# Performance work log

Measured on AMD Instinct MI355X. Metric: run time of the kernel, lower is better.

Reference implementation:

```python
import jax, jax.numpy as jnp
import numpy as np

HEADS = 8
DIM_HEAD = 64
ROT_DIM = DIM_HEAD // 2  # RotaryEmbedding(dim=head_dim//2) rotates first 32 dims of each head
THETA = 10000.0


def _rope_cos_sin(T, dtype):
    # rotary_embedding_torch: freqs = 1/theta**(arange(0,dim,2)/dim), len dim//2,
    # angles repeated interleaved across pairs -> (T, ROT_DIM)
    inv = 1.0 / (THETA ** (jnp.arange(0, ROT_DIM, 2, dtype=jnp.float32) / ROT_DIM))
    ang = jnp.arange(T, dtype=jnp.float32)[:, None] * inv[None, :]      # (T, ROT_DIM/2)
    ang = jnp.repeat(ang, 2, axis=-1)                                   # (T, ROT_DIM) interleaved
    return jnp.cos(ang).astype(dtype), jnp.sin(ang).astype(dtype)


def _rotate_half(x):
    # pairs (x1, x2) -> (-x2, x1), interleaved layout '... (d 2)'
    x = x.reshape(x.shape[:-1] + (-1, 2))
    x = jnp.stack([-x[..., 1], x[..., 0]], axis=-1)
    return x.reshape(x.shape[:-2] + (-1,))


def _apply_rope(x, cos, sin):
    # x: (N, h, T, dh); rotate first ROT_DIM dims, pass through the rest
    xr, xp = x[..., :ROT_DIM], x[..., ROT_DIM:]
    xr = xr * cos[None, None, :, :] + _rotate_half(xr) * sin[None, None, :, :]
    return jnp.concatenate([xr, xp], axis=-1)


def setup_inputs() -> dict:
    key = jax.random.key(0)
    k1, k2, k3 = jax.random.split(key, 3)
    B, T, H, W, D = 2, 32, 32, 32, 512
    inner = HEADS * DIM_HEAD
    x = jax.random.normal(k1, (B, T, H, W, D), dtype=jnp.float32)
    w_qkv = jax.random.normal(k2, (D, 3 * inner), dtype=jnp.float32) * (D ** -0.5)
    w_out = jax.random.normal(k3, (inner, D), dtype=jnp.float32) * (inner ** -0.5)
    b_out = jnp.zeros((D,), dtype=jnp.float32)
    return {"x": x, "w_qkv": w_qkv, "w_out": w_out, "b_out": b_out}


def reference(x, w_qkv, w_out, b_out):
    B, T, H, W, D = x.shape
    qkv = jnp.einsum('bthwd,de->bthwe', x, w_qkv)               # (B,T,H,W,3*inner)
    q, k, v = jnp.split(qkv, 3, axis=-1)

    def to_axial(t):  # (B,T,H,W,inner) -> (B*H*W, heads, T, dh)
        t = t.reshape(B, T, H, W, HEADS, DIM_HEAD)
        t = jnp.transpose(t, (0, 2, 3, 4, 1, 5))
        return t.reshape(B * H * W, HEADS, T, DIM_HEAD)

    q, k, v = to_axial(q), to_axial(k), to_axial(v)
    cos, sin = _rope_cos_sin(T, x.dtype)
    q = _apply_rope(q, cos, sin)
    k = _apply_rope(k, cos, sin)

    scale = DIM_HEAD ** -0.5
    scores = jnp.einsum('nhqd,nhkd->nhqk', q, k) * scale        # (N,h,T,T)
    causal = jnp.tril(jnp.ones((T, T), dtype=bool))
    scores = jnp.where(causal[None, None, :, :], scores, jnp.finfo(scores.dtype).min)
    attn = jax.nn.softmax(scores, axis=-1)
    out = jnp.einsum('nhqk,nhkd->nhqd', attn, v)                # (N,h,T,dh)

    out = out.reshape(B, H, W, HEADS, T, DIM_HEAD)
    out = jnp.transpose(out, (0, 4, 1, 2, 3, 5)).reshape(B, T, H, W, HEADS * DIM_HEAD)
    return jnp.einsum('bthwe,ed->bthwd', out, w_out) + b_out
```

## Files before the change

kernel.cpp:

```cpp
#include <hip/hip_runtime.h>
#include <hip/hip_bf16.h>
#include <math.h>

#define HEADS  8
#define TT     32
#define DMODEL 512
#define HWSZ   1024
#define TSTRIDE (HWSZ*DMODEL)

#define NQKV (3*DMODEL*DMODEL)
#define NOUT (DMODEL*DMODEL)
#define NTAB 512

typedef __attribute__((ext_vector_type(8)))  short bf16x8;
typedef __attribute__((ext_vector_type(4)))  float f32x4;
typedef __attribute__((ext_vector_type(16))) float f32x16;
typedef __attribute__((ext_vector_type(4)))  short s16x4;

__device__ __forceinline__ unsigned short f2bf(float f) {
    unsigned int u = __builtin_bit_cast(unsigned int, f);
    u += 0x7FFFu + ((u >> 16) & 1u);
    return (unsigned short)(u >> 16);
}

__global__ __launch_bounds__(256)
void taa_prep(const float* __restrict__ wqkv, const float* __restrict__ wout,
              unsigned short* __restrict__ ws) {
    long i = (long)blockIdx.x * 256 + threadIdx.x;
    unsigned short* wqf = ws;
    unsigned short* wof = ws + NQKV;
    float* cs = (float*)(wof + NOUT);
    float* sn = cs + NTAB;
    if (i < NQKV) {
        int i8 = (int)(i & 7), lane = (int)((i >> 3) & 63), blk = (int)(i >> 9);
        int k05 = blk & 15, t = blk >> 4;
        int n = t * 16 + (lane & 15);
        int k = k05 * 32 + (lane >> 4) * 8 + i8;
        wqf[i] = f2bf(wqkv[(long)k * 1536 + n]);
    } else if (i < NQKV + NOUT) {
        long j = i - NQKV;
        int i8 = (int)(j & 7), lane = (int)((j >> 3) & 63), blk = (int)(j >> 9);
        int k05 = blk & 15, t = blk >> 4;
        int col = t * 16 + (lane & 15);
        int k = k05 * 32 + (lane >> 4) * 8 + i8;
        wof[j] = f2bf(wout[(long)k * 512 + col]);
    } else if (i < NQKV + NOUT + NTAB) {
        int j = (int)(i - NQKV - NOUT);
        int t = j >> 4, f = j & 15;
        float inv = powf(10000.f, -(float)(2 * f) / 32.f);
        float sv, cv;
        sincosf((float)t * inv, &sv, &cv);
        cs[j] = cv; sn[j] = sv;
    }
}

#define X_OFF  0
#define Q_OFF  65536
#define K_OFF  81920
#define V_OFF  98304
#define PV_OFF 114688
#define CS_OFF 131072
#define SN_OFF 133120
#define LDS_SZ 135168

#define XS(g, r, cB) (X_OFF + ((g) << 15) + ((r) << 10) + ((cB) ^ (((r) & 7) << 4)))
#define RS(base, r, cB) ((base) + ((r) << 7) + ((cB) ^ (((r) & 7) << 4)))
#define VS(base, d, cB) ((base) + ((d) << 6) + ((cB) ^ (((d) & 7) << 3)))

#define MFMA16(a, b, c) __builtin_amdgcn_mfma_f32_16x16x32_bf16((a), (b), (c), 0, 0, 0)
#define MFMA32(a, b, c) __builtin_amdgcn_mfma_f32_32x32x16_bf16((a), (b), (c), 0, 0, 0)

__global__ __launch_bounds__(512, 1)
void taa_main(const float* __restrict__ x,
              const unsigned short* __restrict__ ws,
              const float* __restrict__ b_out,
              float* __restrict__ out) {
    extern __shared__ __align__(16) unsigned char smem[];

    const unsigned short* wqf = ws;
    const unsigned short* wof = ws + NQKV;
    const float* cs_gl = (const float*)(wof + NOUT);
    const float* sn_gl = cs_gl + NTAB;

    const int tid  = threadIdx.x;
    const int lane = tid & 63;
    const int wv   = tid >> 6;
    const int quad = lane >> 4;
    const int lid  = lane & 15;

    const int n0 = blockIdx.x * 2;
    const long long base0 = ((long long)(n0 >> 10) * (TT * HWSZ) + (n0 & 1023)) * DMODEL;
    const int n1 = n0 + 1;
    const long long base1 = ((long long)(n1 >> 10) * (TT * HWSZ) + (n1 & 1023)) * DMODEL;

    float* cs_l = (float*)(smem + CS_OFF);
    float* sn_l = (float*)(smem + SN_OFF);
    for (int i = tid; i < NTAB; i += 512) { cs_l[i] = cs_gl[i]; sn_l[i] = sn_gl[i]; }

    for (int idx = tid; idx < 4096; idx += 512) {
        int g  = idx >> 11;
        int r  = (idx >> 6) & 31;
        int c8 = idx & 63;
        long long bg = g ? base1 : base0;
        const float4* src = (const float4*)(x + bg + (long long)r * TSTRIDE + c8 * 8);
        float4 f0 = src[0], f1 = src[1];
        s16x4 lo, hi;
        lo[0] = (short)f2bf(f0.x); lo[1] = (short)f2bf(f0.y);
        lo[2] = (short)f2bf(f0.z); lo[3] = (short)f2bf(f0.w);
        hi[0] = (short)f2bf(f1.x); hi[1] = (short)f2bf(f1.y);
        hi[2] = (short)f2bf(f1.z); hi[3] = (short)f2bf(f1.w);
        int a = XS(g, r, c8 * 16);
        *(s16x4*)(smem + a)     = lo;
        *(s16x4*)(smem + a + 8) = hi;
    }

    f32x4 oacc[4][2][2];
    #pragma unroll
    for (int j = 0; j < 4; ++j)
        #pragma unroll
        for (int g = 0; g < 2; ++g)
            #pragma unroll
            for (int mt = 0; mt < 2; ++mt) oacc[j][g][mt] = (f32x4){0.f, 0.f, 0.f, 0.f};

    __syncthreads();

    for (int it = 0; it < 4; ++it) {
        const int hpair = it * 2;

        for (int rnd = 0; rnd < 3; ++rnd) {
            int ct  = rnd * 8 + wv;
            int m   = ct >> 3;
            int hh  = (ct >> 2) & 1;
            int t16 = ct & 3;
            int T   = m * 32 + (hpair + hh) * 4 + t16;
            const unsigned short* wp = wqf + ((long)T * 16) * 512 + lane * 8;
            f32x4 acc[2][2];
            #pragma unroll
            for (int g = 0; g < 2; ++g)
                #pragma unroll
                for (int mt = 0; mt < 2; ++mt) acc[g][mt] = (f32x4){0.f, 0.f, 0.f, 0.f};
            #pragma unroll 4
            for (int k05 = 0; k05 < 16; ++k05) {
                bf16x8 bw = *(const bf16x8*)(wp + (long)k05 * 512);
                #pragma unroll
                for (int g = 0; g < 2; ++g)
                    #pragma unroll
                    for (int mt = 0; mt < 2; ++mt) {
                        bf16x8 a = *(const bf16x8*)(smem + XS(g, lid + 16 * mt, k05 * 64 + quad * 16));
                        acc[g][mt] = MFMA16(a, bw, acc[g][mt]);
                    }
            }
            if (m < 2) {
                int dstb = ((m == 0) ? Q_OFF : K_OFF) + hh * 4096;
                if (t16 < 2) {
                    #pragma unroll
                    for (int g = 0; g < 2; ++g)
                        #pragma unroll
                        for (int mt = 0; mt < 2; ++mt)
                            #pragma unroll
                            for (int r = 0; r < 4; ++r) {
                                float v = acc[g][mt][r];
                                float p = __shfl_xor(v, 1, 64);
                                int trow = mt * 16 + quad * 4 + r;
                                int colh = t16 * 16 + lid;
                                int jj = colh >> 1;
                                float cv = cs_l[trow * 16 + jj];
                                float sv = sn_l[trow * 16 + jj];
                                float res = (colh & 1) ? (v * cv + p * sv) : (v * cv - p * sv);
                                *(unsigned short*)(smem + RS(dstb + g * 8192, trow, colh * 2)) = f2bf(res);
                            }
                } else {
                    #pragma unroll
                    for (int g = 0; g < 2; ++g)
                        #pragma unroll
                        for (int mt = 0; mt < 2; ++mt)
                            #pragma unroll
                            for (int r = 0; r < 4; ++r) {
                                int trow = mt * 16 + quad * 4 + r;
                                *(unsigned short*)(smem + RS(dstb + g * 8192, trow, (t16 * 16 + lid) * 2)) = f2bf(acc[g][mt][r]);
                            }
                }
            } else {
                #pragma unroll
                for (int g = 0; g < 2; ++g)
                    #pragma unroll
                    for (int mt = 0; mt < 2; ++mt) {
                        int d  = t16 * 16 + lid;
                        int t0 = mt * 16 + quad * 4;
                        s16x4 pk;
                        pk[0] = (short)f2bf(acc[g][mt][0]); pk[1] = (short)f2bf(acc[g][mt][1]);
                        pk[2] = (short)f2bf(acc[g][mt][2]); pk[3] = (short)f2bf(acc[g][mt][3]);
                        *(s16x4*)(smem + VS(V_OFF + (g * 2 + hh) * 4096, d, t0 * 2)) = pk;
                    }
            }
        }
        __syncthreads();

        {
            int g  = wv >> 2;
            int hh = (wv >> 1) & 1;
            int dt = wv & 1;
            int qr  = Q_OFF  + (g * 2 + hh) * 4096;
            int kr  = K_OFF  + (g * 2 + hh) * 4096;
            int vr  = V_OFF  + (g * 2 + hh) * 4096;
            int pvr = PV_OFF + (g * 2 + hh) * 4096;
            int tq = lane & 31;
            int hf = lane >> 5;

            f32x16 sc = {0.f,0.f,0.f,0.f,0.f,0.f,0.f,0.f,0.f,0.f,0.f,0.f,0.f,0.f,0.f,0.f};
            #pragma unroll
            for (int j = 0; j < 4; ++j) {
                bf16x8 aK = *(const bf16x8*)(smem + RS(kr, tq, j * 32 + hf * 16));
                bf16x8 bQ = *(const bf16x8*)(smem + RS(qr, tq, j * 32 + hf * 16));
                sc = MFMA32(aK, bQ, sc);
            }
            float pe[16];
            float mx = -1e30f;
            #pragma unroll
            for (int r = 0; r < 16; ++r) {
                int tk = (r & 3) + 8 * (r >> 2) + 4 * hf;
                float v = (tk <= tq) ? sc[r] * 0.125f : -1e30f;
                pe[r] = v;
                mx = fmaxf(mx, v);
            }
            mx = fmaxf(mx, __shfl_xor(mx, 32, 64));
            float sum = 0.f;
            #pragma unroll
            for (int r = 0; r < 16; ++r) {
                float e = __expf(pe[r] - mx);
                pe[r] = e;
                sum += e;
            }
            sum += __shfl_xor(sum, 32, 64);
            float inv = 1.f / sum;
            bf16x8 pa0, pa1;
            #pragma unroll
            for (int i = 0; i < 8; ++i) {
                pa0[i] = (short)f2bf(pe[i] * inv);
                pa1[i] = (short)f2bf(pe[8 + i] * inv);
            }
            int d = dt * 32 + tq;
            f32x16 o = {0.f,0.f,0.f,0.f,0.f,0.f,0.f,0.f,0.f,0.f,0.f,0.f,0.f,0.f,0.f,0.f};
            {
                s16x4 lo = *(const s16x4*)(smem + VS(vr, d, 8 * hf));
                s16x4 hi = *(const s16x4*)(smem + VS(vr, d, 16 + 8 * hf));
                bf16x8 bv;
                bv[0] = lo[0]; bv[1] = lo[1]; bv[2] = lo[2]; bv[3] = lo[3];
                bv[4] = hi[0]; bv[5] = hi[1]; bv[6] = hi[2]; bv[7] = hi[3];
                o = MFMA32(pa0, bv, o);
            }
            {
                s16x4 lo = *(const s16x4*)(smem + VS(vr, d, 32 + 8 * hf));
                s16x4 hi = *(const s16x4*)(smem + VS(vr, d, 48 + 8 * hf));
                bf16x8 bv;
                bv[0] = lo[0]; bv[1] = lo[1]; bv[2] = lo[2]; bv[3] = lo[3];
                bv[4] = hi[0]; bv[5] = hi[1]; bv[6] = hi[2]; bv[7] = hi[3];
                o = MFMA32(pa1, bv, o);
            }
            #pragma unroll
            for (int r = 0; r < 16; ++r) {
                int t = (r & 3) + 8 * (r >> 2) + 4 * hf;
                *(unsigned short*)(smem + RS(pvr, t, 2 * d)) = f2bf(o[r]);
            }
        }
        __syncthreads();

        {
            #pragma unroll
            for (int k05h = 0; k05h < 4; ++k05h) {
                int hh   = k05h >> 1;
                int dblk = k05h & 1;
                int kb   = (hpair + hh) * 2 + dblk;
                bf16x8 a[2][2];
                #pragma unroll
                for (int g = 0; g < 2; ++g)
                    #pragma unroll
                    for (int mt = 0; mt < 2; ++mt)
                        a[g][mt] = *(const bf16x8*)(smem + RS(PV_OFF + (g * 2 + hh) * 4096, lid + 16 * mt, dblk * 64 + quad * 16));
                #pragma unroll
                for (int j = 0; j < 4; ++j) {
                    int ct = wv + 8 * j;
                    bf16x8 bw = *(const bf16x8*)(wof + ((long)(ct * 16 + kb)) * 512 + lane * 8);
                    #pragma unroll
                    for (int g = 0; g < 2; ++g)
                        #pragma unroll
                        for (int mt = 0; mt < 2; ++mt)
                            oacc[j][g][mt] = MFMA16(a[g][mt], bw, oacc[j][g][mt]);
                }
            }
        }
    }

    #pragma unroll
    for (int j = 0; j < 4; ++j) {
        int col = (wv + 8 * j) * 16 + lid;
        float bias = b_out[col];
        #pragma unroll
        for (int g = 0; g < 2; ++g) {
            long long bg = g ? base1 : base0;
            #pragma unroll
            for (int mt = 0; mt < 2; ++mt)
                #pragma unroll
                for (int r = 0; r < 4; ++r) {
                    int t = mt * 16 + quad * 4 + r;
                    out[bg + (long long)t * TSTRIDE + col] = oacc[j][g][mt][r] + bias;
                }
        }
    }
}

extern "C" void kernel_launch(void* const* d_in, const int* in_sizes, int n_in,
                              void* d_out, int out_size, void* d_ws, size_t ws_size,
                              hipStream_t stream) {
    const float* x     = (const float*)d_in[0];
    const float* w_qkv = (const float*)d_in[1];
    const float* w_out = (const float*)d_in[2];
    const float* b_out = (const float*)d_in[3];
    float* out = (float*)d_out;
    (void)in_sizes; (void)n_in; (void)out_size; (void)ws_size;

    unsigned short* ws = (unsigned short*)d_ws;

    taa_prep<<<dim3(4098), dim3(256), 0, stream>>>(w_qkv, w_out, ws);
    taa_main<<<dim3(1024), dim3(512), LDS_SZ, stream>>>(x, ws, b_out, out);
}
```

Baseline: 239.4 us.

## Switch QKV and output projections to 32x32 MFMA with per-wave head ownership

The QKV and output projections move from 16x16x32 MFMA tiles to 32x32x16 MFMA tiles, and the prepacked weight layout changes to match. Each wave now computes Q, K and V for one head, sample and d-half, sharing one A-fragment load across three MFMAs. Work is no longer spread over three rounds of mixed tiles. The PV buffer is relaid so the output projection reads a contiguous 32-row tile, and the launch-bounds occupancy hint rises to 2. The aim is fewer LDS A-operand loads per MFMA and less per-round bookkeeping, at the cost of larger f32x16 accumulators and more register pressure.

```diff
diff --git a/kernel.cpp b/kernel.cpp
--- a/kernel.cpp
+++ b/kernel.cpp
@@ -13,7 +13,6 @@
 #define NTAB 512
 
 typedef __attribute__((ext_vector_type(8)))  short bf16x8;
-typedef __attribute__((ext_vector_type(4)))  float f32x4;
 typedef __attribute__((ext_vector_type(16))) float f32x16;
 typedef __attribute__((ext_vector_type(4)))  short s16x4;
 
@@ -21,6 +20,11 @@
     unsigned int u = __builtin_bit_cast(unsigned int, f);
     u += 0x7FFFu + ((u >> 16) & 1u);
     return (unsigned short)(u >> 16);
+}
+
+__device__ __forceinline__ f32x16 fz16() {
+    f32x16 v = {0.f,0.f,0.f,0.f,0.f,0.f,0.f,0.f,0.f,0.f,0.f,0.f,0.f,0.f,0.f,0.f};
+    return v;
 }
 
 __global__ __launch_bounds__(256)
@@ -33,17 +37,17 @@
     float* sn = cs + NTAB;
     if (i < NQKV) {
         int i8 = (int)(i & 7), lane = (int)((i >> 3) & 63), blk = (int)(i >> 9);
-        int k05 = blk & 15, t = blk >> 4;
-        int n = t * 16 + (lane & 15);
-        int k = k05 * 32 + (lane >> 4) * 8 + i8;
+        int ks = blk & 31, ct = blk >> 5;
+        int n = ct * 32 + (lane & 31);
+        int k = ks * 16 + (lane >> 5) * 8 + i8;
         wqf[i] = f2bf(wqkv[(long)k * 1536 + n]);
     } else if (i < NQKV + NOUT) {
         long j = i - NQKV;
         int i8 = (int)(j & 7), lane = (int)((j >> 3) & 63), blk = (int)(j >> 9);
-        int k05 = blk & 15, t = blk >> 4;
-        int col = t * 16 + (lane & 15);
-        int k = k05 * 32 + (lane >> 4) * 8 + i8;
-        wof[j] = f2bf(wout[(long)k * 512 + col]);
+        int ks = blk & 31, ct = blk >> 5;
+        int n = ct * 32 + (lane & 31);
+        int k = ks * 16 + (lane >> 5) * 8 + i8;
+        wof[j] = f2bf(wout[(long)k * 512 + n]);
     } else if (i < NQKV + NOUT + NTAB) {
         int j = (int)(i - NQKV - NOUT);
         int t = j >> 4, f = j & 15;
@@ -63,14 +67,14 @@
 #define SN_OFF 133120
 #define LDS_SZ 135168
 
-#define XS(g, r, cB) (X_OFF + ((g) << 15) + ((r) << 10) + ((cB) ^ (((r) & 7) << 4)))
-#define RS(base, r, cB) ((base) + ((r) << 7) + ((cB) ^ (((r) & 7) << 4)))
-#define VS(base, d, cB) ((base) + ((d) << 6) + ((cB) ^ (((d) & 7) << 3)))
-
-#define MFMA16(a, b, c) __builtin_amdgcn_mfma_f32_16x16x32_bf16((a), (b), (c), 0, 0, 0)
+#define XS(g,r,cB) (X_OFF + ((g)<<15) + ((r)<<10) + ((cB) ^ (((r)&7)<<4)))
+#define RS(base,r,cB) ((base) + ((r)<<7) + ((cB) ^ (((r)&7)<<4)))
+#define VS(base,d,cB) ((base) + ((d)<<6) + ((cB) ^ (((d)&7)<<3)))
+#define PS(g,r,cB) (PV_OFF + ((g)<<13) + ((r)<<8) + ((cB) ^ (((r)&7)<<4)))
+
 #define MFMA32(a, b, c) __builtin_amdgcn_mfma_f32_32x32x16_bf16((a), (b), (c), 0, 0, 0)
 
-__global__ __launch_bounds__(512, 1)
+__global__ __launch_bounds__(512, 2)
 void taa_main(const float* __restrict__ x,
               const unsigned short* __restrict__ ws,
               const float* __restrict__ b_out,
@@ -85,8 +89,8 @@
     const int tid  = threadIdx.x;
     const int lane = tid & 63;
     const int wv   = tid >> 6;
-    const int quad = lane >> 4;
-    const int lid  = lane & 15;
+    const int hf   = lane >> 5;
+    const int tq   = lane & 31;
 
     const int n0 = blockIdx.x * 2;
     const long long base0 = ((long long)(n0 >> 10) * (TT * HWSZ) + (n0 & 1023)) * DMODEL;
@@ -114,100 +118,76 @@
         *(s16x4*)(smem + a + 8) = hi;
     }
 
-    f32x4 oacc[4][2][2];
-    #pragma unroll
-    for (int j = 0; j < 4; ++j)
-        #pragma unroll
-        for (int g = 0; g < 2; ++g)
-            #pragma unroll
-            for (int mt = 0; mt < 2; ++mt) oacc[j][g][mt] = (f32x4){0.f, 0.f, 0.f, 0.f};
+    f32x16 oac[2][2];
+    oac[0][0] = fz16(); oac[0][1] = fz16();
+    oac[1][0] = fz16(); oac[1][1] = fz16();
 
     __syncthreads();
 
+    const int g  = wv >> 2;
+    const int hh = (wv >> 1) & 1;
+    const int dh = wv & 1;
+
     for (int it = 0; it < 4; ++it) {
-        const int hpair = it * 2;
-
-        for (int rnd = 0; rnd < 3; ++rnd) {
-            int ct  = rnd * 8 + wv;
-            int m   = ct >> 3;
-            int hh  = (ct >> 2) & 1;
-            int t16 = ct & 3;
-            int T   = m * 32 + (hpair + hh) * 4 + t16;
-            const unsigned short* wp = wqf + ((long)T * 16) * 512 + lane * 8;
-            f32x4 acc[2][2];
-            #pragma unroll
-            for (int g = 0; g < 2; ++g)
+        const int hd = it * 2 + hh;
+
+        const unsigned short* pq = wqf + ((long)((      hd * 2 + dh) * 32)) * 512 + lane * 8;
+        const unsigned short* pk = wqf + ((long)((16 + hd * 2 + dh) * 32)) * 512 + lane * 8;
+        const unsigned short* pv = wqf + ((long)((32 + hd * 2 + dh) * 32)) * 512 + lane * 8;
+        f32x16 aq = fz16(), ak = fz16(), av = fz16();
+        #pragma unroll 4
+        for (int ks = 0; ks < 32; ++ks) {
+            bf16x8 a   = *(const bf16x8*)(smem + XS(g, tq, ks * 32 + hf * 16));
+            bf16x8 wq_ = *(const bf16x8*)(pq + (long)ks * 512);
+            bf16x8 wk_ = *(const bf16x8*)(pk + (long)ks * 512);
+            bf16x8 wv_ = *(const bf16x8*)(pv + (long)ks * 512);
+            aq = MFMA32(a, wq_, aq);
+            ak = MFMA32(a, wk_, ak);
+            av = MFMA32(a, wv_, av);
+        }
+        {
+            int qb = Q_OFF + (g * 2 + hh) * 4096;
+            int kb = K_OFF + (g * 2 + hh) * 4096;
+            if (dh == 0) {
                 #pragma unroll
-                for (int mt = 0; mt < 2; ++mt) acc[g][mt] = (f32x4){0.f, 0.f, 0.f, 0.f};
-            #pragma unroll 4
-            for (int k05 = 0; k05 < 16; ++k05) {
-                bf16x8 bw = *(const bf16x8*)(wp + (long)k05 * 512);
-                #pragma unroll
-                for (int g = 0; g < 2; ++g)
-                    #pragma unroll
-                    for (int mt = 0; mt < 2; ++mt) {
-                        bf16x8 a = *(const bf16x8*)(smem + XS(g, lid + 16 * mt, k05 * 64 + quad * 16));
-                        acc[g][mt] = MFMA16(a, bw, acc[g][mt]);
-                    }
-            }
-            if (m < 2) {
-                int dstb = ((m == 0) ? Q_OFF : K_OFF) + hh * 4096;
-                if (t16 < 2) {
-                    #pragma unroll
-                    for (int g = 0; g < 2; ++g)
-                        #pragma unroll
-                        for (int mt = 0; mt < 2; ++mt)
-                            #pragma unroll
-                            for (int r = 0; r < 4; ++r) {
-                                float v = acc[g][mt][r];
-                                float p = __shfl_xor(v, 1, 64);
-                                int trow = mt * 16 + quad * 4 + r;
-                                int colh = t16 * 16 + lid;
-                                int jj = colh >> 1;
-                                float cv = cs_l[trow * 16 + jj];
-                                float sv = sn_l[trow * 16 + jj];
-                                float res = (colh & 1) ? (v * cv + p * sv) : (v * cv - p * sv);
-                                *(unsigned short*)(smem + RS(dstb + g * 8192, trow, colh * 2)) = f2bf(res);
-                            }
-                } else {
-                    #pragma unroll
-                    for (int g = 0; g < 2; ++g)
-                        #pragma unroll
-                        for (int mt = 0; mt < 2; ++mt)
-                            #pragma unroll
-                            for (int r = 0; r < 4; ++r) {
-                                int trow = mt * 16 + quad * 4 + r;
-                                *(unsigned short*)(smem + RS(dstb + g * 8192, trow, (t16 * 16 + lid) * 2)) = f2bf(acc[g][mt][r]);
-                            }
+                for (int r = 0; r < 16; ++r) {
+                    int t = (r & 3) + 8 * (r >> 2) + 4 * hf;
+                    float cv = cs_l[t * 16 + (tq >> 1)];
+                    float sv = sn_l[t * 16 + (tq >> 1)];
+                    float vq = aq[r], pq2 = __shfl_xor(vq, 1, 64);
+                    float rq = (tq & 1) ? (vq * cv + pq2 * sv) : (vq * cv - pq2 * sv);
+                    *(unsigned short*)(smem + RS(qb, t, tq * 2)) = f2bf(rq);
+                    float vk = ak[r], pk2 = __shfl_xor(vk, 1, 64);
+                    float rk = (tq & 1) ? (vk * cv + pk2 * sv) : (vk * cv - pk2 * sv);
+                    *(unsigned short*)(smem + RS(kb, t, tq * 2)) = f2bf(rk);
                 }
             } else {
                 #pragma unroll
-                for (int g = 0; g < 2; ++g)
-                    #pragma unroll
-                    for (int mt = 0; mt < 2; ++mt) {
-                        int d  = t16 * 16 + lid;
-                        int t0 = mt * 16 + quad * 4;
-                        s16x4 pk;
-                        pk[0] = (short)f2bf(acc[g][mt][0]); pk[1] = (short)f2bf(acc[g][mt][1]);
-                        pk[2] = (short)f2bf(acc[g][mt][2]); pk[3] = (short)f2bf(acc[g][mt][3]);
-                        *(s16x4*)(smem + VS(V_OFF + (g * 2 + hh) * 4096, d, t0 * 2)) = pk;
-                    }
+                for (int r = 0; r < 16; ++r) {
+                    int t = (r & 3) + 8 * (r >> 2) + 4 * hf;
+                    *(unsigned short*)(smem + RS(qb, t, 64 + tq * 2)) = f2bf(aq[r]);
+                    *(unsigned short*)(smem + RS(kb, t, 64 + tq * 2)) = f2bf(ak[r]);
+                }
+            }
+            int vb = V_OFF + (g * 2 + hh) * 4096;
+            int d  = dh * 32 + tq;
+            #pragma unroll
+            for (int c = 0; c < 4; ++c) {
+                s16x4 pkk;
+                pkk[0] = (short)f2bf(av[c * 4 + 0]);
+                pkk[1] = (short)f2bf(av[c * 4 + 1]);
+                pkk[2] = (short)f2bf(av[c * 4 + 2]);
+                pkk[3] = (short)f2bf(av[c * 4 + 3]);
+                *(s16x4*)(smem + VS(vb, d, c * 16 + hf * 8)) = pkk;
             }
         }
         __syncthreads();
 
         {
-            int g  = wv >> 2;
-            int hh = (wv >> 1) & 1;
-            int dt = wv & 1;
-            int qr  = Q_OFF  + (g * 2 + hh) * 4096;
-            int kr  = K_OFF  + (g * 2 + hh) * 4096;
-            int vr  = V_OFF  + (g * 2 + hh) * 4096;
-            int pvr = PV_OFF + (g * 2 + hh) * 4096;
-            int tq = lane & 31;
-            int hf = lane >> 5;
-
-            f32x16 sc = {0.f,0.f,0.f,0.f,0.f,0.f,0.f,0.f,0.f,0.f,0.f,0.f,0.f,0.f,0.f,0.f};
+            int qr = Q_OFF + (g * 2 + hh) * 4096;
+            int kr = K_OFF + (g * 2 + hh) * 4096;
+            int vr = V_OFF + (g * 2 + hh) * 4096;
+            f32x16 sc = fz16();
             #pragma unroll
             for (int j = 0; j < 4; ++j) {
                 bf16x8 aK = *(const bf16x8*)(smem + RS(kr, tq, j * 32 + hf * 16));
@@ -235,12 +215,12 @@
             float inv = 1.f / sum;
             bf16x8 pa0, pa1;
             #pragma unroll
-            for (int i = 0; i < 8; ++i) {
-                pa0[i] = (short)f2bf(pe[i] * inv);
-                pa1[i] = (short)f2bf(pe[8 + i] * inv);
-            }
-            int d = dt * 32 + tq;
-            f32x16 o = {0.f,0.f,0.f,0.f,0.f,0.f,0.f,0.f,0.f,0.f,0.f,0.f,0.f,0.f,0.f,0.f};
+            for (int i2 = 0; i2 < 8; ++i2) {
+                pa0[i2] = (short)f2bf(pe[i2] * inv);
+                pa1[i2] = (short)f2bf(pe[8 + i2] * inv);
+            }
+            int d = dh * 32 + tq;
+            f32x16 o = fz16();
             {
                 s16x4 lo = *(const s16x4*)(smem + VS(vr, d, 8 * hf));
                 s16x4 hi = *(const s16x4*)(smem + VS(vr, d, 16 + 8 * hf));
@@ -260,51 +240,39 @@
             #pragma unroll
             for (int r = 0; r < 16; ++r) {
                 int t = (r & 3) + 8 * (r >> 2) + 4 * hf;
-                *(unsigned short*)(smem + RS(pvr, t, 2 * d)) = f2bf(o[r]);
+                *(unsigned short*)(smem + PS(g, t, (hh * 64 + d) * 2)) = f2bf(o[r]);
             }
         }
         __syncthreads();
 
         {
             #pragma unroll
-            for (int k05h = 0; k05h < 4; ++k05h) {
-                int hh   = k05h >> 1;
-                int dblk = k05h & 1;
-                int kb   = (hpair + hh) * 2 + dblk;
-                bf16x8 a[2][2];
-                #pragma unroll
-                for (int g = 0; g < 2; ++g)
-                    #pragma unroll
-                    for (int mt = 0; mt < 2; ++mt)
-                        a[g][mt] = *(const bf16x8*)(smem + RS(PV_OFF + (g * 2 + hh) * 4096, lid + 16 * mt, dblk * 64 + quad * 16));
-                #pragma unroll
-                for (int j = 0; j < 4; ++j) {
-                    int ct = wv + 8 * j;
-                    bf16x8 bw = *(const bf16x8*)(wof + ((long)(ct * 16 + kb)) * 512 + lane * 8);
-                    #pragma unroll
-                    for (int g = 0; g < 2; ++g)
-                        #pragma unroll
-                        for (int mt = 0; mt < 2; ++mt)
-                            oacc[j][g][mt] = MFMA16(a[g][mt], bw, oacc[j][g][mt]);
-                }
+            for (int ksl = 0; ksl < 8; ++ksl) {
+                int ksg = it * 8 + ksl;
+                bf16x8 a0 = *(const bf16x8*)(smem + PS(0, tq, ksl * 32 + hf * 16));
+                bf16x8 a1 = *(const bf16x8*)(smem + PS(1, tq, ksl * 32 + hf * 16));
+                bf16x8 b0 = *(const bf16x8*)(wof + ((long)(wv * 32 + ksg)) * 512 + lane * 8);
+                bf16x8 b1 = *(const bf16x8*)(wof + ((long)((wv + 8) * 32 + ksg)) * 512 + lane * 8);
+                oac[0][0] = MFMA32(a0, b0, oac[0][0]);
+                oac[0][1] = MFMA32(a1, b0, oac[0][1]);
+                oac[1][0] = MFMA32(a0, b1, oac[1][0]);
+                oac[1][1] = MFMA32(a1, b1, oac[1][1]);
             }
         }
     }
 
     #pragma unroll
-    for (int j = 0; j < 4; ++j) {
-        int col = (wv + 8 * j) * 16 + lid;
-        float bias = b_out[col];
+    for (int jj = 0; jj < 2; ++jj) {
+        int coln = (wv + 8 * jj) * 32 + tq;
+        float bias = b_out[coln];
         #pragma unroll
-        for (int g = 0; g < 2; ++g) {
-            long long bg = g ? base1 : base0;
-            #pragma unroll
-            for (int mt = 0; mt < 2; ++mt)
-                #pragma unroll
-                for (int r = 0; r < 4; ++r) {
-                    int t = mt * 16 + quad * 4 + r;
-                    out[bg + (long long)t * TSTRIDE + col] = oacc[j][g][mt][r] + bias;
-                }
+        for (int gg = 0; gg < 2; ++gg) {
+            long long bg = gg ? base1 : base0;
+            #pragma unroll
+            for (int r = 0; r < 16; ++r) {
+                int t = (r & 3) + 8 * (r >> 2) + 4 * hf;
+                out[bg + (long long)t * TSTRIDE + coln] = oac[jj][gg][r] + bias;
+            }
         }
     }
 }
```

Measured after the change: 347.5 us. 45.1% more time.

## Stage bf16 X tile in global scratch to halve LDS and fit two blocks

Applied to the files above, without the earlier changes.

When the workspace is large enough, each block writes its bf16-converted input tile to a global scratch buffer in MFMA-fragment order instead of LDS. The QKV projection then reads A operands from global memory, which are likely cached in L2. Dropping this tile cuts LDS from about 132KB to 68KB, and launch bounds change to allow two 512-thread blocks per CU for more latency hiding. The cost is extra global write and read traffic, plus a possible read-after-write visibility gap within the block, since no fence sits between the global stores and the later loads beyond __syncthreads.

```diff
diff --git a/kernel.cpp b/kernel.cpp
--- a/kernel.cpp
+++ b/kernel.cpp
@@ -11,6 +11,9 @@
 #define NQKV (3*DMODEL*DMODEL)
 #define NOUT (DMODEL*DMODEL)
 #define NTAB 512
+#define XF_OFF_SHORTS (NQKV + NOUT + 2048)
+#define XF_BYTES      ((size_t)2048 * 16384 * 2)
+#define WS_NEED       ((size_t)XF_OFF_SHORTS * 2 + XF_BYTES)
 
 typedef __attribute__((ext_vector_type(8)))  short bf16x8;
 typedef __attribute__((ext_vector_type(4)))  float f32x4;
@@ -21,6 +24,11 @@
     unsigned int u = __builtin_bit_cast(unsigned int, f);
     u += 0x7FFFu + ((u >> 16) & 1u);
     return (unsigned short)(u >> 16);
+}
+
+__device__ __forceinline__ f32x16 fz16() {
+    f32x16 v = {0.f,0.f,0.f,0.f,0.f,0.f,0.f,0.f,0.f,0.f,0.f,0.f,0.f,0.f,0.f,0.f};
+    return v;
 }
 
 __global__ __launch_bounds__(256)
@@ -54,28 +62,28 @@
     }
 }
 
-#define X_OFF  0
-#define Q_OFF  65536
-#define K_OFF  81920
-#define V_OFF  98304
-#define PV_OFF 114688
-#define CS_OFF 131072
-#define SN_OFF 133120
-#define LDS_SZ 135168
-
-#define XS(g, r, cB) (X_OFF + ((g) << 15) + ((r) << 10) + ((cB) ^ (((r) & 7) << 4)))
-#define RS(base, r, cB) ((base) + ((r) << 7) + ((cB) ^ (((r) & 7) << 4)))
-#define VS(base, d, cB) ((base) + ((d) << 6) + ((cB) ^ (((d) & 7) << 3)))
+#define RS(base,r,cB) ((base) + ((r)<<7) + ((cB) ^ (((r)&7)<<4)))
+#define VS(base,d,cB) ((base) + ((d)<<6) + ((cB) ^ (((d)&7)<<3)))
 
 #define MFMA16(a, b, c) __builtin_amdgcn_mfma_f32_16x16x32_bf16((a), (b), (c), 0, 0, 0)
 #define MFMA32(a, b, c) __builtin_amdgcn_mfma_f32_32x32x16_bf16((a), (b), (c), 0, 0, 0)
 
-__global__ __launch_bounds__(512, 1)
+template<bool XF>
+__global__ __launch_bounds__(512, 2)
 void taa_main(const float* __restrict__ x,
               const unsigned short* __restrict__ ws,
               const float* __restrict__ b_out,
-              float* __restrict__ out) {
+              float* __restrict__ out,
+              unsigned short* __restrict__ xf) {
     extern __shared__ __align__(16) unsigned char smem[];
+
+    constexpr int XO  = 0;
+    constexpr int QO  = XF ? 0 : 65536;
+    constexpr int KO  = QO + 16384;
+    constexpr int VO  = KO + 16384;
+    constexpr int PO  = VO + 16384;
+    constexpr int CSO = PO + 16384;
+    constexpr int SNO = CSO + 2048;
 
     const unsigned short* wqf = ws;
     const unsigned short* wof = ws + NQKV;
@@ -93,8 +101,8 @@
     const int n1 = n0 + 1;
     const long long base1 = ((long long)(n1 >> 10) * (TT * HWSZ) + (n1 & 1023)) * DMODEL;
 
-    float* cs_l = (float*)(smem + CS_OFF);
-    float* sn_l = (float*)(smem + SN_OFF);
+    float* cs_l = (float*)(smem + CSO);
+    float* sn_l = (float*)(smem + SNO);
     for (int i = tid; i < NTAB; i += 512) { cs_l[i] = cs_gl[i]; sn_l[i] = sn_gl[i]; }
 
     for (int idx = tid; idx < 4096; idx += 512) {
@@ -109,9 +117,17 @@
         lo[2] = (short)f2bf(f0.z); lo[3] = (short)f2bf(f0.w);
         hi[0] = (short)f2bf(f1.x); hi[1] = (short)f2bf(f1.y);
         hi[2] = (short)f2bf(f1.z); hi[3] = (short)f2bf(f1.w);
-        int a = XS(g, r, c8 * 16);
-        *(s16x4*)(smem + a)     = lo;
-        *(s16x4*)(smem + a + 8) = hi;
+        if constexpr (XF) {
+            unsigned short* dst = xf + (long)(n0 + g) * 16384
+                                + (((r >> 4) * 16 + (c8 >> 2)) * 64
+                                   + ((r & 15) + (c8 & 3) * 16)) * 8;
+            *(s16x4*)dst       = lo;
+            *(s16x4*)(dst + 4) = hi;
+        } else {
+            int a = XO + (g << 15) + (r << 10) + ((c8 * 16) ^ (((r) & 7) << 4));
+            *(s16x4*)(smem + a)     = lo;
+            *(s16x4*)(smem + a + 8) = hi;
+        }
     }
 
     f32x4 oacc[4][2][2];
@@ -146,12 +162,19 @@
                 for (int g = 0; g < 2; ++g)
                     #pragma unroll
                     for (int mt = 0; mt < 2; ++mt) {
-                        bf16x8 a = *(const bf16x8*)(smem + XS(g, lid + 16 * mt, k05 * 64 + quad * 16));
+                        bf16x8 a;
+                        if constexpr (XF)
+                            a = *(const bf16x8*)(xf + (long)(n0 + g) * 16384
+                                                 + ((mt * 16 + k05) * 64 + lane) * 8);
+                        else
+                            a = *(const bf16x8*)(smem + XO + (g << 15)
+                                                 + ((lid + 16 * mt) << 10)
+                                                 + ((k05 * 64 + quad * 16) ^ (((lid + 16 * mt) & 7) << 4)));
                         acc[g][mt] = MFMA16(a, bw, acc[g][mt]);
                     }
             }
             if (m < 2) {
-                int dstb = ((m == 0) ? Q_OFF : K_OFF) + hh * 4096;
+                int dstb = ((m == 0) ? QO : KO) + hh * 4096;
                 if (t16 < 2) {
                     #pragma unroll
                     for (int g = 0; g < 2; ++g)
@@ -190,7 +213,7 @@
                         s16x4 pk;
                         pk[0] = (short)f2bf(acc[g][mt][0]); pk[1] = (short)f2bf(acc[g][mt][1]);
                         pk[2] = (short)f2bf(acc[g][mt][2]); pk[3] = (short)f2bf(acc[g][mt][3]);
-                        *(s16x4*)(smem + VS(V_OFF + (g * 2 + hh) * 4096, d, t0 * 2)) = pk;
+                        *(s16x4*)(smem + VS(VO + (g * 2 + hh) * 4096, d, t0 * 2)) = pk;
                     }
             }
         }
@@ -200,14 +223,14 @@
             int g  = wv >> 2;
             int hh = (wv >> 1) & 1;
             int dt = wv & 1;
-            int qr  = Q_OFF  + (g * 2 + hh) * 4096;
-            int kr  = K_OFF  + (g * 2 + hh) * 4096;
-            int vr  = V_OFF  + (g * 2 + hh) * 4096;
-            int pvr = PV_OFF + (g * 2 + hh) * 4096;
+            int qr  = QO + (g * 2 + hh) * 4096;
+            int kr  = KO + (g * 2 + hh) * 4096;
+            int vr  = VO + (g * 2 + hh) * 4096;
+            int pvr = PO + (g * 2 + hh) * 4096;
             int tq = lane & 31;
             int hf = lane >> 5;
 
-            f32x16 sc = {0.f,0.f,0.f,0.f,0.f,0.f,0.f,0.f,0.f,0.f,0.f,0.f,0.f,0.f,0.f,0.f};
+            f32x16 sc = fz16();
             #pragma unroll
             for (int j = 0; j < 4; ++j) {
                 bf16x8 aK = *(const bf16x8*)(smem + RS(kr, tq, j * 32 + hf * 16));
@@ -235,12 +258,12 @@
             float inv = 1.f / sum;
             bf16x8 pa0, pa1;
             #pragma unroll
-            for (int i = 0; i < 8; ++i) {
-                pa0[i] = (short)f2bf(pe[i] * inv);
-                pa1[i] = (short)f2bf(pe[8 + i] * inv);
+            for (int i2 = 0; i2 < 8; ++i2) {
+                pa0[i2] = (short)f2bf(pe[i2] * inv);
+                pa1[i2] = (short)f2bf(pe[8 + i2] * inv);
             }
             int d = dt * 32 + tq;
-            f32x16 o = {0.f,0.f,0.f,0.f,0.f,0.f,0.f,0.f,0.f,0.f,0.f,0.f,0.f,0.f,0.f,0.f};
+            f32x16 o = fz16();
             {
                 s16x4 lo = *(const s16x4*)(smem + VS(vr, d, 8 * hf));
                 s16x4 hi = *(const s16x4*)(smem + VS(vr, d, 16 + 8 * hf));
@@ -276,7 +299,7 @@
                 for (int g = 0; g < 2; ++g)
                     #pragma unroll
                     for (int mt = 0; mt < 2; ++mt)
-                        a[g][mt] = *(const bf16x8*)(smem + RS(PV_OFF + (g * 2 + hh) * 4096, lid + 16 * mt, dblk * 64 + quad * 16));
+                        a[g][mt] = *(const bf16x8*)(smem + RS(PO + (g * 2 + hh) * 4096, lid + 16 * mt, dblk * 64 + quad * 16));
                 #pragma unroll
                 for (int j = 0; j < 4; ++j) {
                     int ct = wv + 8 * j;
@@ -317,10 +340,15 @@
     const float* w_out = (const float*)d_in[2];
     const float* b_out = (const float*)d_in[3];
     float* out = (float*)d_out;
-    (void)in_sizes; (void)n_in; (void)out_size; (void)ws_size;
+    (void)in_sizes; (void)n_in; (void)out_size;
 
     unsigned short* ws = (unsigned short*)d_ws;
 
     taa_prep<<<dim3(4098), dim3(256), 0, stream>>>(w_qkv, w_out, ws);
-    taa_main<<<dim3(1024), dim3(512), LDS_SZ, stream>>>(x, ws, b_out, out);
-}
+    if (ws_size >= WS_NEED) {
+        unsigned short* xf = ws + XF_OFF_SHORTS;
+        taa_main<true><<<dim3(1024), dim3(512), 69632, stream>>>(x, ws, b_out, out, xf);
+    } else {
+        taa_main<false><<<dim3(1024), dim3(512), 135168, stream>>>(x, ws, b_out, out, nullptr);
+    }
+}
```

New measurement: 385.5 us. 61.0% more time.
